# Performance work log

Measured on AMD Instinct MI355X. Metric: run time of the kernel, lower is better.

The kernel has to match this reference:

```python
import jax, jax.numpy as jnp
import numpy as np

NUM_HEADS = 12
HEAD_DIM = 64
HIDDEN = 768
SLOT_DIM = 30
BS = 8
FULL = SLOT_DIM * BS  # 240
SLOT_LEN = 32
LEN0 = 512   # slot-broadcast cache length
LEN1 = 128   # per-sample cache length


def tf_slot(x, slot_dim):
    # (slot_dim*bs, H, L, h) -> (bs, H, slot_dim*L, h)
    full, nh, L, h = x.shape
    bs = full // slot_dim
    x = x.reshape(slot_dim, bs, nh, L, h).transpose(1, 2, 0, 3, 4)
    return x.reshape(bs, nh, slot_dim * L, h)


def back_slot(x, slot_dim):
    # (bs, H, slot_dim*L, h) -> (slot_dim*bs, H, L, h)
    bs, nh, total, h = x.shape
    L = total // slot_dim
    x = x.reshape(bs, nh, slot_dim, L, h).transpose(2, 0, 1, 3, 4)
    return x.reshape(slot_dim * bs, nh, L, h)


def setup_inputs() -> dict:
    key = jax.random.key(0)
    ks = jax.random.split(key, 12)
    s = 0.02
    return {
        "hidden_states": jax.random.normal(ks[0], (FULL, SLOT_LEN, HIDDEN), jnp.float32),
        "attention_mask": jnp.zeros((FULL, 1, 1, LEN0 + LEN1 + SLOT_LEN), jnp.float32),
        "cache0_key": jax.random.normal(ks[1], (BS, NUM_HEADS, LEN0, HEAD_DIM), jnp.float32),
        "cache0_value": jax.random.normal(ks[2], (BS, NUM_HEADS, LEN0, HEAD_DIM), jnp.float32),
        "cache1_key": jax.random.normal(ks[3], (FULL, NUM_HEADS, LEN1, HEAD_DIM), jnp.float32),
        "cache1_value": jax.random.normal(ks[4], (FULL, NUM_HEADS, LEN1, HEAD_DIM), jnp.float32),
        "Wq": jax.random.normal(ks[5], (HIDDEN, HIDDEN), jnp.float32) * s,
        "bq": jax.random.normal(ks[6], (HIDDEN,), jnp.float32) * s,
        "Wk": jax.random.normal(ks[7], (HIDDEN, HIDDEN), jnp.float32) * s,
        "bk": jax.random.normal(ks[8], (HIDDEN,), jnp.float32) * s,
        "Wv": jax.random.normal(ks[9], (HIDDEN, HIDDEN), jnp.float32) * s,
        "bv": jax.random.normal(ks[10], (HIDDEN,), jnp.float32) * s,
        "slot_dim": SLOT_DIM,
    }


def reference(hidden_states, attention_mask, cache0_key, cache0_value,
              cache1_key, cache1_value, Wq, bq, Wk, bk, Wv, bv, slot_dim):
    B, L, hid = hidden_states.shape

    def split_heads(x):  # (B, L, hid) -> (B, H, L, h)
        return x.reshape(B, L, NUM_HEADS, HEAD_DIM).transpose(0, 2, 1, 3)

    q = split_heads(hidden_states @ Wq + bq)
    k = split_heads(hidden_states @ Wk + bk)
    v = split_heads(hidden_states @ Wv + bv)

    # self-attention scores (B, H, L, L)
    self_scores = jnp.einsum('bhqd,bhkd->bhqk', q, k)

    # cache0: slot-broadcast path (cache batch = bs, queries batch = slot_dim*bs)
    q_tf = tf_slot(q, slot_dim)  # (bs, H, slot_dim*L, h)
    s0 = back_slot(jnp.einsum('bhqd,bhkd->bhqk', q_tf, cache0_key), slot_dim)  # (B,H,L,LEN0)
    # cache1: direct path (matching batch)
    s1 = jnp.einsum('bhqd,bhkd->bhqk', q, cache1_key)  # (B,H,L,LEN1)

    scores = jnp.concatenate([s0, s1, self_scores], axis=-1)
    scores = scores / jnp.sqrt(jnp.float32(HEAD_DIM)) + attention_mask
    probs = jax.nn.softmax(scores, axis=-1)  # single softmax over all KV sources

    len0 = cache0_key.shape[2]
    len1 = cache1_key.shape[2]
    # self context
    ctx = jnp.einsum('bhqk,bhkd->bhqd', probs[..., -L:], v)
    # cache0 context via slot transform
    p0 = tf_slot(probs[..., :len0], slot_dim)  # (bs, H, slot_dim*L, LEN0)
    ctx = ctx + back_slot(jnp.einsum('bhqk,bhkd->bhqd', p0, cache0_value), slot_dim)
    # cache1 context direct
    ctx = ctx + jnp.einsum('bhqk,bhkd->bhqd', probs[..., len0:len0 + len1], cache1_value)

    # (B, H, L, h) -> (B, L, hid)
    return ctx.transpose(0, 2, 1, 3).reshape(B, L, hid)
```

## Files before the change

kernel.cpp:

```cpp
#include <hip/hip_runtime.h>
#include <math.h>

#define NUM_HEADS 12
#define HEAD_DIM  64
#define HIDDEN    768
#define BS        8
#define FULL      240
#define SLOT_LEN  32
#define LEN0      512
#define LEN1      128
#define KTOT      672
#define M_TOK     (FULL * SLOT_LEN)

typedef float f32x4 __attribute__((ext_vector_type(4)));
typedef short s16x8 __attribute__((ext_vector_type(8)));
typedef short s16x4 __attribute__((ext_vector_type(4)));

__device__ __forceinline__ short f2bf(float x) {
    unsigned u = __float_as_uint(x);
    unsigned r = (u + 0x7fffu + ((u >> 16) & 1u)) >> 16;
    return (short)r;
}

__global__ __launch_bounds__(256) void cast_hs(const float* __restrict__ in,
                                               short* __restrict__ out, int n4) {
    int i = blockIdx.x * 256 + threadIdx.x;
    if (i < n4) {
        float4 v = ((const float4*)in)[i];
        s16x4 o = {f2bf(v.x), f2bf(v.y), f2bf(v.z), f2bf(v.w)};
        ((s16x4*)out)[i] = o;
    }
}

__global__ __launch_bounds__(256) void cast_w_t(const float* __restrict__ Wq,
                                                const float* __restrict__ Wk,
                                                const float* __restrict__ Wv,
                                                short* __restrict__ WtAll) {
    const float* W = (blockIdx.z == 0) ? Wq : (blockIdx.z == 1) ? Wk : Wv;
    short* Wt = WtAll + (size_t)blockIdx.z * HIDDEN * HIDDEN;
    __shared__ __align__(16) float tile[32][33];
    const int kb0 = blockIdx.y * 32, nb0 = blockIdx.x * 32;
    const int r = threadIdx.x >> 3, c4 = (threadIdx.x & 7) * 4;
    float4 v = *(const float4*)&W[(size_t)(kb0 + r) * HIDDEN + nb0 + c4];
    tile[r][c4 + 0] = v.x; tile[r][c4 + 1] = v.y;
    tile[r][c4 + 2] = v.z; tile[r][c4 + 3] = v.w;
    __syncthreads();
    s16x4 o = {f2bf(tile[c4 + 0][r]), f2bf(tile[c4 + 1][r]),
               f2bf(tile[c4 + 2][r]), f2bf(tile[c4 + 3][r])};
    *(s16x4*)&Wt[(size_t)(nb0 + r) * HIDDEN + kb0 + c4] = o;
}

__global__ __launch_bounds__(256) void qkv_mfma(
    const short* __restrict__ hsb, const short* __restrict__ WtAll,
    const float* __restrict__ bq, const float* __restrict__ bk,
    const float* __restrict__ bv,
    short* __restrict__ qo, short* __restrict__ ko, short* __restrict__ vo)
{
    const int z = blockIdx.z;
    const short* Wt = WtAll + (size_t)z * HIDDEN * HIDDEN;
    const float* bias = (z == 0) ? bq : (z == 1) ? bk : bv;
    short* outp = (z == 0) ? qo : (z == 1) ? ko : vo;

    __shared__ __align__(16) short smem[2 * 128 * 72];
    short* As = smem;
    short* Bs = smem + 128 * 72;

    const int t = threadIdx.x;
    const int lane = t & 63, w = t >> 6;
    const int l15 = lane & 15, quad = lane >> 4;
    const int mBase = blockIdx.y * 128, nBase = blockIdx.x * 128;
    const int mw = (w & 1) * 64, nw = (w >> 1) * 64;

    f32x4 acc[4][4];
    const f32x4 z4 = {0.f, 0.f, 0.f, 0.f};
#pragma unroll
    for (int i = 0; i < 4; ++i)
#pragma unroll
        for (int j = 0; j < 4; ++j) acc[i][j] = z4;

    for (int kb = 0; kb < HIDDEN; kb += 64) {
        __syncthreads();
#pragma unroll
        for (int j = 0; j < 4; ++j) {
            int u = t + j * 256;
            int row = u >> 3, kc8 = (u & 7) * 8;
            *(s16x8*)&As[row * 72 + kc8] =
                *(const s16x8*)&hsb[(size_t)(mBase + row) * HIDDEN + kb + kc8];
            *(s16x8*)&Bs[row * 72 + kc8] =
                *(const s16x8*)&Wt[(size_t)(nBase + row) * HIDDEN + kb + kc8];
        }
        __syncthreads();
#pragma unroll
        for (int kc = 0; kc < 2; ++kc) {
            const int ko2 = kc * 32 + quad * 8;
            s16x8 a[4], b[4];
#pragma unroll
            for (int mt = 0; mt < 4; ++mt)
                a[mt] = *(const s16x8*)&As[(mw + mt * 16 + l15) * 72 + ko2];
#pragma unroll
            for (int nt = 0; nt < 4; ++nt)
                b[nt] = *(const s16x8*)&Bs[(nw + nt * 16 + l15) * 72 + ko2];
#pragma unroll
            for (int mt = 0; mt < 4; ++mt)
#pragma unroll
                for (int nt = 0; nt < 4; ++nt)
                    acc[mt][nt] = __builtin_amdgcn_mfma_f32_16x16x32_bf16(
                        a[mt], b[nt], acc[mt][nt], 0, 0, 0);
        }
    }

    __syncthreads();
#pragma unroll
    for (int nt = 0; nt < 4; ++nt) {
        float bvv = bias[nBase + nw + nt * 16 + l15];
        int col = nw + nt * 16 + l15;
#pragma unroll
        for (int mt = 0; mt < 4; ++mt)
#pragma unroll
            for (int r = 0; r < 4; ++r) {
                int row = mw + mt * 16 + quad * 4 + r;
                smem[row * 128 + col] = f2bf(acc[mt][nt][r] + bvv);
            }
    }
    __syncthreads();
#pragma unroll
    for (int i = 0; i < 8; ++i) {
        int f = t + i * 256;
        int row = f >> 4, c8 = (f & 15) * 8;
        uint4 val = *(const uint4*)&smem[row * 128 + c8];
        int m = mBase + row, n = nBase + c8;
        size_t dst = (((size_t)(m >> 5) * NUM_HEADS + (n >> 6)) * SLOT_LEN + (m & 31)) * 64 + (n & 63);
        *(uint4*)&outp[dst] = val;
    }
}

__global__ __launch_bounds__(256) void attn_mfma(
    const short* __restrict__ qb, const short* __restrict__ kbuf,
    const short* __restrict__ vbuf,
    const float* __restrict__ c0k, const float* __restrict__ c0v,
    const float* __restrict__ c1k, const float* __restrict__ c1v,
    const float* __restrict__ mask, float* __restrict__ out)
{
    __shared__ __align__(16) short Klds[4][32][72];
    __shared__ __align__(16) short Vt[4][64][44];
    __shared__ __align__(16) short Plds[4][32][40];

    const int t = threadIdx.x, lane = t & 63, w = t >> 6;
    const int task = blockIdx.x * 4 + w;
    const int B = task / 12, h = task % 12;
    const int l15 = lane & 15, quad = lane >> 4;

    const short* qp  = qb  + (size_t)(B * NUM_HEADS + h) * SLOT_LEN * 64;
    const short* ksp = kbuf + (size_t)(B * NUM_HEADS + h) * SLOT_LEN * 64;
    const short* vsp = vbuf + (size_t)(B * NUM_HEADS + h) * SLOT_LEN * 64;
    const float* k0p = c0k + (size_t)((B & 7) * NUM_HEADS + h) * LEN0 * 64;
    const float* v0p = c0v + (size_t)((B & 7) * NUM_HEADS + h) * LEN0 * 64;
    const float* k1p = c1k + (size_t)(B * NUM_HEADS + h) * LEN1 * 64;
    const float* v1p = c1v + (size_t)(B * NUM_HEADS + h) * LEN1 * 64;
    const float* mp  = mask + (size_t)B * KTOT;

    short (*K)[72] = Klds[w];
    short (*V)[44] = Vt[w];
    short (*P)[40] = Plds[w];

    s16x8 qf[2][2];
#pragma unroll
    for (int qh = 0; qh < 2; ++qh)
#pragma unroll
        for (int kc = 0; kc < 2; ++kc)
            qf[qh][kc] = *(const s16x8*)&qp[(qh * 16 + l15) * 64 + kc * 32 + quad * 8];

    const f32x4 z4 = {0.f, 0.f, 0.f, 0.f};
    f32x4 o[2][4];
    float lpart[2][4];
#pragma unroll
    for (int qh = 0; qh < 2; ++qh) {
#pragma unroll
        for (int dq = 0; dq < 4; ++dq) o[qh][dq] = z4;
#pragma unroll
        for (int r = 0; r < 4; ++r) lpart[qh][r] = 0.f;
    }

    for (int c = 0; c < 21; ++c) {
        if (c < 20) {
            const float* sk; const float* sv;
            if (c < 16) { sk = k0p + c * 32 * 64;        sv = v0p + c * 32 * 64; }
            else        { sk = k1p + (c - 16) * 32 * 64; sv = v1p + (c - 16) * 32 * 64; }
#pragma unroll
            for (int i = 0; i < 8; ++i) {
                int f = i * 64 + lane;
                int key = f >> 4, c4 = (f & 15) << 2;
                float4 kv = *(const float4*)&sk[key * 64 + c4];
                float4 vv = *(const float4*)&sv[key * 64 + c4];
                s16x4 kk = {f2bf(kv.x), f2bf(kv.y), f2bf(kv.z), f2bf(kv.w)};
                *(s16x4*)&K[key][c4] = kk;
                V[c4 + 0][key] = f2bf(vv.x);
                V[c4 + 1][key] = f2bf(vv.y);
                V[c4 + 2][key] = f2bf(vv.z);
                V[c4 + 3][key] = f2bf(vv.w);
            }
        } else {
#pragma unroll
            for (int i = 0; i < 8; ++i) {
                int f = i * 64 + lane;
                int key = f >> 4, c4 = (f & 15) << 2;
                s16x4 kk = *(const s16x4*)&ksp[key * 64 + c4];
                s16x4 vv = *(const s16x4*)&vsp[key * 64 + c4];
                *(s16x4*)&K[key][c4] = kk;
                V[c4 + 0][key] = vv[0];
                V[c4 + 1][key] = vv[1];
                V[c4 + 2][key] = vv[2];
                V[c4 + 3][key] = vv[3];
            }
        }

        f32x4 s[2][2];
#pragma unroll
        for (int qh = 0; qh < 2; ++qh)
#pragma unroll
            for (int kh = 0; kh < 2; ++kh) s[qh][kh] = z4;
#pragma unroll
        for (int kh = 0; kh < 2; ++kh) {
            s16x8 kf0 = *(const s16x8*)&K[kh * 16 + l15][quad * 8];
            s16x8 kf1 = *(const s16x8*)&K[kh * 16 + l15][32 + quad * 8];
#pragma unroll
            for (int qh = 0; qh < 2; ++qh) {
                s[qh][kh] = __builtin_amdgcn_mfma_f32_16x16x32_bf16(qf[qh][0], kf0, s[qh][kh], 0, 0, 0);
                s[qh][kh] = __builtin_amdgcn_mfma_f32_16x16x32_bf16(qf[qh][1], kf1, s[qh][kh], 0, 0, 0);
            }
        }

        const float mv0 = mp[c * 32 + l15];
        const float mv1 = mp[c * 32 + 16 + l15];

#pragma unroll
        for (int qh = 0; qh < 2; ++qh)
#pragma unroll
            for (int kh = 0; kh < 2; ++kh) {
                float mv = kh ? mv1 : mv0;
#pragma unroll
                for (int r = 0; r < 4; ++r) {
                    float p = __expf(s[qh][kh][r] * 0.125f + mv);
                    lpart[qh][r] += p;
                    P[qh * 16 + quad * 4 + r][kh * 16 + l15] = f2bf(p);
                }
            }

#pragma unroll
        for (int qh = 0; qh < 2; ++qh) {
            s16x4 plo = *(const s16x4*)&P[qh * 16 + l15][quad * 8];
            s16x4 phi = *(const s16x4*)&P[qh * 16 + l15][quad * 8 + 4];
            s16x8 pf = __builtin_shufflevector(plo, phi, 0, 1, 2, 3, 4, 5, 6, 7);
#pragma unroll
            for (int dq = 0; dq < 4; ++dq) {
                s16x4 vlo = *(const s16x4*)&V[dq * 16 + l15][quad * 8];
                s16x4 vhi = *(const s16x4*)&V[dq * 16 + l15][quad * 8 + 4];
                s16x8 vf = __builtin_shufflevector(vlo, vhi, 0, 1, 2, 3, 4, 5, 6, 7);
                o[qh][dq] = __builtin_amdgcn_mfma_f32_16x16x32_bf16(pf, vf, o[qh][dq], 0, 0, 0);
            }
        }
    }

    float linv[2][4];
#pragma unroll
    for (int qh = 0; qh < 2; ++qh)
#pragma unroll
        for (int r = 0; r < 4; ++r) {
            float l = lpart[qh][r];
            l += __shfl_xor(l, 1);
            l += __shfl_xor(l, 2);
            l += __shfl_xor(l, 4);
            l += __shfl_xor(l, 8);
            linv[qh][r] = 1.f / l;
        }

#pragma unroll
    for (int qh = 0; qh < 2; ++qh)
#pragma unroll
        for (int dq = 0; dq < 4; ++dq)
#pragma unroll
            for (int r = 0; r < 4; ++r) {
                int row = qh * 16 + quad * 4 + r;
                out[((size_t)B * SLOT_LEN + row) * HIDDEN + h * 64 + dq * 16 + l15] =
                    o[qh][dq][r] * linv[qh][r];
            }
}

extern "C" void kernel_launch(void* const* d_in, const int* in_sizes, int n_in,
                              void* d_out, int out_size, void* d_ws, size_t ws_size,
                              hipStream_t stream) {
    const float* hs   = (const float*)d_in[0];
    const float* mask = (const float*)d_in[1];
    const float* c0k  = (const float*)d_in[2];
    const float* c0v  = (const float*)d_in[3];
    const float* c1k  = (const float*)d_in[4];
    const float* c1v  = (const float*)d_in[5];
    const float* Wq   = (const float*)d_in[6];
    const float* bq   = (const float*)d_in[7];
    const float* Wk   = (const float*)d_in[8];
    const float* bk   = (const float*)d_in[9];
    const float* Wv   = (const float*)d_in[10];
    const float* bv   = (const float*)d_in[11];
    float* out = (float*)d_out;

    short* hsb = (short*)d_ws;
    short* WtA = hsb + (size_t)M_TOK * HIDDEN;
    short* qb  = WtA + (size_t)3 * HIDDEN * HIDDEN;
    short* kbw = qb + (size_t)M_TOK * HIDDEN;
    short* vbw = kbw + (size_t)M_TOK * HIDDEN;

    cast_hs<<<(M_TOK * HIDDEN / 4 + 255) / 256, 256, 0, stream>>>(hs, hsb, M_TOK * HIDDEN / 4);
    cast_w_t<<<dim3(24, 24, 3), 256, 0, stream>>>(Wq, Wk, Wv, WtA);
    qkv_mfma<<<dim3(HIDDEN / 128, M_TOK / 128, 3), 256, 0, stream>>>(
        hsb, WtA, bq, bk, bv, qb, kbw, vbw);
    attn_mfma<<<720, 256, 0, stream>>>(qb, kbw, vbw, c0k, c0v, c1k, c1v, mask, out);
}
```

Before: 401.7 us.

## Prefetch next tiles into registers in QKV GEMM and attention loops

```diff
diff --git a/kernel.cpp b/kernel.cpp
--- a/kernel.cpp
+++ b/kernel.cpp
@@ -50,7 +50,7 @@
     *(s16x4*)&Wt[(size_t)(nb0 + r) * HIDDEN + kb0 + c4] = o;
 }
 
-__global__ __launch_bounds__(256) void qkv_mfma(
+__global__ __launch_bounds__(256, 3) void qkv_mfma(
     const short* __restrict__ hsb, const short* __restrict__ WtAll,
     const float* __restrict__ bq, const float* __restrict__ bk,
     const float* __restrict__ bv,
@@ -70,6 +70,7 @@
     const int l15 = lane & 15, quad = lane >> 4;
     const int mBase = blockIdx.y * 128, nBase = blockIdx.x * 128;
     const int mw = (w & 1) * 64, nw = (w >> 1) * 64;
+    const int srow = t >> 3, skc8 = (t & 7) * 8;
 
     f32x4 acc[4][4];
     const f32x4 z4 = {0.f, 0.f, 0.f, 0.f};
@@ -78,18 +79,28 @@
 #pragma unroll
         for (int j = 0; j < 4; ++j) acc[i][j] = z4;
 
+    uint4 pa[4], pb[4];
+#pragma unroll
+    for (int j = 0; j < 4; ++j) {
+        pa[j] = *(const uint4*)&hsb[(size_t)(mBase + srow + j * 32) * HIDDEN + skc8];
+        pb[j] = *(const uint4*)&Wt[(size_t)(nBase + srow + j * 32) * HIDDEN + skc8];
+    }
+
     for (int kb = 0; kb < HIDDEN; kb += 64) {
         __syncthreads();
 #pragma unroll
         for (int j = 0; j < 4; ++j) {
-            int u = t + j * 256;
-            int row = u >> 3, kc8 = (u & 7) * 8;
-            *(s16x8*)&As[row * 72 + kc8] =
-                *(const s16x8*)&hsb[(size_t)(mBase + row) * HIDDEN + kb + kc8];
-            *(s16x8*)&Bs[row * 72 + kc8] =
-                *(const s16x8*)&Wt[(size_t)(nBase + row) * HIDDEN + kb + kc8];
+            *(uint4*)&As[(srow + j * 32) * 72 + skc8] = pa[j];
+            *(uint4*)&Bs[(srow + j * 32) * 72 + skc8] = pb[j];
         }
         __syncthreads();
+        if (kb + 64 < HIDDEN) {
+#pragma unroll
+            for (int j = 0; j < 4; ++j) {
+                pa[j] = *(const uint4*)&hsb[(size_t)(mBase + srow + j * 32) * HIDDEN + kb + 64 + skc8];
+                pb[j] = *(const uint4*)&Wt[(size_t)(nBase + srow + j * 32) * HIDDEN + kb + 64 + skc8];
+            }
+        }
 #pragma unroll
         for (int kc = 0; kc < 2; ++kc) {
             const int ko2 = kc * 32 + quad * 8;
@@ -134,7 +145,7 @@
     }
 }
 
-__global__ __launch_bounds__(256) void attn_mfma(
+__global__ __launch_bounds__(256, 3) void attn_mfma(
     const short* __restrict__ qb, const short* __restrict__ kbuf,
     const short* __restrict__ vbuf,
     const float* __restrict__ c0k, const float* __restrict__ c0v,
@@ -142,8 +153,8 @@
     const float* __restrict__ mask, float* __restrict__ out)
 {
     __shared__ __align__(16) short Klds[4][32][72];
-    __shared__ __align__(16) short Vt[4][64][44];
-    __shared__ __align__(16) short Plds[4][32][40];
+    __shared__ __align__(16) short Vt[4][64][36];
+    __shared__ __align__(16) short Plds[4][32][36];
 
     const int t = threadIdx.x, lane = t & 63, w = t >> 6;
     const int task = blockIdx.x * 4 + w;
@@ -160,8 +171,8 @@
     const float* mp  = mask + (size_t)B * KTOT;
 
     short (*K)[72] = Klds[w];
-    short (*V)[44] = Vt[w];
-    short (*P)[40] = Plds[w];
+    short (*V)[36] = Vt[w];
+    short (*P)[36] = Plds[w];
 
     s16x8 qf[2][2];
 #pragma unroll
@@ -181,38 +192,68 @@
         for (int r = 0; r < 4; ++r) lpart[qh][r] = 0.f;
     }
 
+    float4 kreg[8];
+    float  vreg[32];
+    float  mreg0, mreg1;
+
+    auto issue_loads = [&](int c) {
+        const float* sk = (c < 16) ? k0p + c * 2048 : k1p + (c - 16) * 2048;
+        const float* sv = (c < 16) ? v0p + c * 2048 : v1p + (c - 16) * 2048;
+#pragma unroll
+        for (int i = 0; i < 8; ++i) {
+            int f = i * 64 + lane;
+            kreg[i] = *(const float4*)&sk[(f >> 4) * 64 + ((f & 15) << 2)];
+        }
+#pragma unroll
+        for (int key = 0; key < 32; ++key)
+            vreg[key] = sv[key * 64 + lane];
+    };
+    auto issue_mask = [&](int c) {
+        mreg0 = mp[c * 32 + l15];
+        mreg1 = mp[c * 32 + 16 + l15];
+    };
+    auto write_lds = [&]() {
+#pragma unroll
+        for (int i = 0; i < 8; ++i) {
+            int f = i * 64 + lane;
+            int key = f >> 4, c4 = (f & 15) << 2;
+            s16x4 kk = {f2bf(kreg[i].x), f2bf(kreg[i].y), f2bf(kreg[i].z), f2bf(kreg[i].w)};
+            *(s16x4*)&K[key][c4] = kk;
+        }
+#pragma unroll
+        for (int k4 = 0; k4 < 8; ++k4) {
+            s16x4 vv = {f2bf(vreg[k4 * 4 + 0]), f2bf(vreg[k4 * 4 + 1]),
+                        f2bf(vreg[k4 * 4 + 2]), f2bf(vreg[k4 * 4 + 3])};
+            *(s16x4*)&V[lane][k4 * 4] = vv;
+        }
+    };
+
+    issue_loads(0);
+    issue_mask(0);
+
     for (int c = 0; c < 21; ++c) {
         if (c < 20) {
-            const float* sk; const float* sv;
-            if (c < 16) { sk = k0p + c * 32 * 64;        sv = v0p + c * 32 * 64; }
-            else        { sk = k1p + (c - 16) * 32 * 64; sv = v1p + (c - 16) * 32 * 64; }
+            write_lds();
+        } else {
 #pragma unroll
             for (int i = 0; i < 8; ++i) {
                 int f = i * 64 + lane;
                 int key = f >> 4, c4 = (f & 15) << 2;
-                float4 kv = *(const float4*)&sk[key * 64 + c4];
-                float4 vv = *(const float4*)&sv[key * 64 + c4];
-                s16x4 kk = {f2bf(kv.x), f2bf(kv.y), f2bf(kv.z), f2bf(kv.w)};
-                *(s16x4*)&K[key][c4] = kk;
-                V[c4 + 0][key] = f2bf(vv.x);
-                V[c4 + 1][key] = f2bf(vv.y);
-                V[c4 + 2][key] = f2bf(vv.z);
-                V[c4 + 3][key] = f2bf(vv.w);
-            }
-        } else {
-#pragma unroll
-            for (int i = 0; i < 8; ++i) {
-                int f = i * 64 + lane;
-                int key = f >> 4, c4 = (f & 15) << 2;
-                s16x4 kk = *(const s16x4*)&ksp[key * 64 + c4];
-                s16x4 vv = *(const s16x4*)&vsp[key * 64 + c4];
-                *(s16x4*)&K[key][c4] = kk;
-                V[c4 + 0][key] = vv[0];
-                V[c4 + 1][key] = vv[1];
-                V[c4 + 2][key] = vv[2];
-                V[c4 + 3][key] = vv[3];
-            }
-        }
+                *(s16x4*)&K[key][c4] = *(const s16x4*)&ksp[key * 64 + c4];
+            }
+            short vtmp[32];
+#pragma unroll
+            for (int key = 0; key < 32; ++key) vtmp[key] = vsp[key * 64 + lane];
+#pragma unroll
+            for (int k4 = 0; k4 < 8; ++k4) {
+                s16x4 vv = {vtmp[k4 * 4 + 0], vtmp[k4 * 4 + 1],
+                            vtmp[k4 * 4 + 2], vtmp[k4 * 4 + 3]};
+                *(s16x4*)&V[lane][k4 * 4] = vv;
+            }
+        }
+        const float mv0 = mreg0, mv1 = mreg1;
+        if (c + 1 < 20) issue_loads(c + 1);
+        if (c + 1 < 21) issue_mask(c + 1);
 
         f32x4 s[2][2];
 #pragma unroll
@@ -229,9 +270,6 @@
                 s[qh][kh] = __builtin_amdgcn_mfma_f32_16x16x32_bf16(qf[qh][1], kf1, s[qh][kh], 0, 0, 0);
             }
         }
-
-        const float mv0 = mp[c * 32 + l15];
-        const float mv1 = mp[c * 32 + 16 + l15];
 
 #pragma unroll
         for (int qh = 0; qh < 2; ++qh)
```

Measured after the change: 475.2 us. +18.3%, slower.
